# Kernel optimization log

Measured on AMD Instinct MI355X. Metric: run time of the kernel, lower is better.

The kernel has to match this reference:

```python
import jax, jax.numpy as jnp
import numpy as np

N, D, E = 100000, 128, 1600000
BN_EPS = 1e-5

def setup_inputs() -> dict:
    key = jax.random.key(0)
    k1, k2, k3 = jax.random.split(key, 3)
    src_embeddings = jax.random.normal(k1, (N, D), dtype=jnp.float32)
    dst_embeddings = jax.random.normal(k2, (N, D), dtype=jnp.float32)
    graph = jax.random.randint(k3, (2, E), 0, N, dtype=jnp.int64)
    bn_weight = jnp.ones((1,), dtype=jnp.float32)
    bn_bias = jnp.zeros((1,), dtype=jnp.float32)
    return {
        "src_embeddings": src_embeddings,
        "dst_embeddings": dst_embeddings,
        "graph": graph,
        "bn_weight": bn_weight,
        "bn_bias": bn_bias,
    }

def reference(src_embeddings, dst_embeddings, graph, bn_weight, bn_bias):
    # gather endpoint embeddings by edge indices: [E, D]
    src = src_embeddings[graph[0]]
    dst = dst_embeddings[graph[1]]
    # squared distance per edge, clamped as in torch .clamp(min=1e-12)
    d2 = jnp.clip(jnp.sum((src - dst) ** 2, axis=-1), 1e-12, None)  # [E]
    likelihood = -jnp.log(d2)
    # BatchNorm1d(1) in training mode: batch mean, biased variance, eps=1e-5
    mu = jnp.mean(likelihood)
    var = jnp.mean((likelihood - mu) ** 2)
    edge_weights_logits = bn_weight[0] * (likelihood - mu) * jax.lax.rsqrt(var + BN_EPS) + bn_bias[0]
    # weighting_function = torch.sigmoid
    edge_weights = jax.nn.sigmoid(edge_weights_logits)
    # normalize=True: divide by mean
    edge_weights = edge_weights / jnp.mean(edge_weights)
    edge_weights = edge_weights[:, None]  # [E, 1]
    return graph, edge_weights, edge_weights_logits
```

## Files before the change

### kernel.cpp

```cpp
#include <hip/hip_runtime.h>
#include <math.h>

#define EMB_D 128
#define BN_EPS 1e-5f

#define QSCALE 22.0f
#define INV_QS2 (1.0f / (QSCALE * QSCALE))

typedef float v4f __attribute__((ext_vector_type(4)));

#if defined(__has_builtin)
#if __has_builtin(__builtin_amdgcn_sdot4)
#define SDOT4_HW 1
#endif
#endif

__device__ __forceinline__ int sdot4i(unsigned int a, unsigned int b, int c) {
#ifdef SDOT4_HW
    return __builtin_amdgcn_sdot4((int)a, (int)b, c, false);
#else
    int s = c;
    s += (((int)a << 24) >> 24) * (((int)b << 24) >> 24);
    s += (((int)a << 16) >> 24) * (((int)b << 16) >> 24);
    s += (((int)a << 8)  >> 24) * (((int)b << 8)  >> 24);
    s += ((int)a >> 24) * ((int)b >> 24);
    return s;
#endif
}

__device__ __forceinline__ unsigned int q4(float4 v) {
    const int a = (int)rintf(fminf(fmaxf(v.x * QSCALE, -127.0f), 127.0f));
    const int b = (int)rintf(fminf(fmaxf(v.y * QSCALE, -127.0f), 127.0f));
    const int c = (int)rintf(fminf(fmaxf(v.z * QSCALE, -127.0f), 127.0f));
    const int d = (int)rintf(fminf(fmaxf(v.w * QSCALE, -127.0f), 127.0f));
    return (unsigned int)(a & 0xff) | ((unsigned int)(b & 0xff) << 8)
         | ((unsigned int)(c & 0xff) << 16) | ((unsigned int)(d & 0xff) << 24);
}

__device__ __forceinline__ float n4(float4 v) {
    return fmaf(v.x, v.x, fmaf(v.y, v.y, fmaf(v.z, v.z, v.w * v.w)));
}

__global__ void prep_kernel(const float* __restrict__ src,
                            const float* __restrict__ dst,
                            uint4* __restrict__ src8,
                            uint4* __restrict__ dst8,
                            float* __restrict__ nsrc,
                            float* __restrict__ ndst,
                            long long N,
                            const int* __restrict__ g,
                            long long E,
                            float* __restrict__ out_graph)
{
    const int sub = threadIdx.x & 7;
    const int grp = threadIdx.x >> 3;
    const long long rstride = (long long)gridDim.x * 32;

    for (long long r = (long long)blockIdx.x * 32 + grp; r < N; r += rstride) {
        const float4* rp = (const float4*)(src + r * EMB_D) + sub * 4;
        const float4 x0 = rp[0], x1 = rp[1], x2 = rp[2], x3 = rp[3];
        uint4 w;
        w.x = q4(x0); w.y = q4(x1); w.z = q4(x2); w.w = q4(x3);
        src8[r * 8 + sub] = w;
        float nrm = n4(x0) + n4(x1) + n4(x2) + n4(x3);
        nrm += __shfl_xor(nrm, 1, 64);
        nrm += __shfl_xor(nrm, 2, 64);
        nrm += __shfl_xor(nrm, 4, 64);
        if (sub == 0) nsrc[r] = nrm;
    }
    for (long long r = (long long)blockIdx.x * 32 + grp; r < N; r += rstride) {
        const float4* rp = (const float4*)(dst + r * EMB_D) + sub * 4;
        const float4 x0 = rp[0], x1 = rp[1], x2 = rp[2], x3 = rp[3];
        uint4 w;
        w.x = q4(x0); w.y = q4(x1); w.z = q4(x2); w.w = q4(x3);
        dst8[r * 8 + sub] = w;
        float nrm = n4(x0) + n4(x1) + n4(x2) + n4(x3);
        nrm += __shfl_xor(nrm, 1, 64);
        nrm += __shfl_xor(nrm, 2, 64);
        nrm += __shfl_xor(nrm, 4, 64);
        if (sub == 0) ndst[r] = nrm;
    }

    const long long nthreads = (long long)gridDim.x * blockDim.x;
    const long long tid0 = (long long)blockIdx.x * blockDim.x + threadIdx.x;
    const long long gvec = (2 * E) / 4;
    for (long long i = tid0; i < gvec; i += nthreads) {
        const int4 v = ((const int4*)g)[i];
        v4f f;
        f.x = (float)v.x; f.y = (float)v.y; f.z = (float)v.z; f.w = (float)v.w;
        __builtin_nontemporal_store(f, (v4f*)out_graph + i);
    }
    for (long long i = gvec * 4 + tid0; i < 2 * E; i += nthreads)
        out_graph[i] = (float)g[i];
}

__global__ void edge_l_i8_kernel(const uint4* __restrict__ src8,
                                 const uint4* __restrict__ dst8,
                                 const int* __restrict__ g,
                                 long long E,
                                 const float* __restrict__ nsrc,
                                 const float* __restrict__ ndst,
                                 float* __restrict__ l_out,
                                 double* __restrict__ acc)
{
    const int tid = threadIdx.x;
    const int sub = tid & 7;
    const int grp = tid >> 3;
    const long long blkSpan = 64;
    const long long stride = (long long)gridDim.x * blkSpan;

    double sumL = 0.0, sumL2 = 0.0;

    for (long long base = (long long)blockIdx.x * blkSpan; base < E; base += stride) {
        const long long e1 = base + (long long)grp * 2;
        const long long e2 = e1 + 1;
        const bool ok1 = e1 < E;
        const bool ok2 = e2 < E;

        int s1 = 0, d1 = 0, s2 = 0, d2i = 0;
        if (ok1) { s1 = g[e1]; d1 = g[E + e1]; }
        if (ok2) { s2 = g[e2]; d2i = g[E + e2]; }

        const uint4 A1 = src8[(long long)s1 * 8 + sub];
        const uint4 B1 = dst8[(long long)d1 * 8 + sub];
        const uint4 A2 = src8[(long long)s2 * 8 + sub];
        const uint4 B2 = dst8[(long long)d2i * 8 + sub];

        int p1 = sdot4i(A1.x, B1.x, 0);
        p1 = sdot4i(A1.y, B1.y, p1);
        p1 = sdot4i(A1.z, B1.z, p1);
        p1 = sdot4i(A1.w, B1.w, p1);
        int p2 = sdot4i(A2.x, B2.x, 0);
        p2 = sdot4i(A2.y, B2.y, p2);
        p2 = sdot4i(A2.z, B2.z, p2);
        p2 = sdot4i(A2.w, B2.w, p2);

        p1 += __shfl_xor(p1, 1, 64);
        p1 += __shfl_xor(p1, 2, 64);
        p1 += __shfl_xor(p1, 4, 64);
        p2 += __shfl_xor(p2, 1, 64);
        p2 += __shfl_xor(p2, 2, 64);
        p2 += __shfl_xor(p2, 4, 64);

        if (sub == 0) {
            if (ok1) {
                const float d2 = nsrc[s1] + ndst[d1]
                               - 2.0f * (float)p1 * INV_QS2;
                const float L = -logf(fmaxf(d2, 1e-12f));
                l_out[e1] = L;
                sumL  += (double)L;
                sumL2 += (double)L * (double)L;
            }
            if (ok2) {
                const float d2 = nsrc[s2] + ndst[d2i]
                               - 2.0f * (float)p2 * INV_QS2;
                const float L = -logf(fmaxf(d2, 1e-12f));
                l_out[e2] = L;
                sumL  += (double)L;
                sumL2 += (double)L * (double)L;
            }
        }
    }

    __shared__ double sA[256];
    __shared__ double sB[256];
    sA[tid] = sumL;
    sB[tid] = sumL2;
    __syncthreads();
    for (int ofs = 128; ofs >= 1; ofs >>= 1) {
        if (tid < ofs) {
            sA[tid] += sA[tid + ofs];
            sB[tid] += sB[tid + ofs];
        }
        __syncthreads();
    }
    if (tid == 0) {
        atomicAdd(&acc[0], sA[0]);
        atomicAdd(&acc[1], sB[0]);
    }
}

__global__ void edge_l_kernel(const float* __restrict__ src,
                              const float* __restrict__ dst,
                              const int*   __restrict__ g,
                              long long E,
                              float*  __restrict__ l_out,
                              double* __restrict__ acc)
{
    const int sub  = threadIdx.x & 7;
    const int egrp = threadIdx.x >> 3;
    const long long stride = (long long)gridDim.x * 32;

    double sumL = 0.0, sumL2 = 0.0;

    long long e = (long long)blockIdx.x * 32 + egrp;
    int s = 0, d = 0;
    if (e < E) { s = g[e]; d = g[E + e]; }

    while (e < E) {
        const long long en = e + stride;
        int sn = 0, dn = 0;
        if (en < E) { sn = g[en]; dn = g[E + en]; }

        const float4* sa = (const float4*)(src + (long long)s * EMB_D);
        const float4* sb = (const float4*)(dst + (long long)d * EMB_D);
        const float4 a0 = sa[sub];      const float4 b0 = sb[sub];
        const float4 a1 = sa[sub + 8];  const float4 b1 = sb[sub + 8];
        const float4 a2 = sa[sub + 16]; const float4 b2 = sb[sub + 16];
        const float4 a3 = sa[sub + 24]; const float4 b3 = sb[sub + 24];

        float dx, dy, dz, dw, p = 0.f;
        dx = a0.x-b0.x; dy = a0.y-b0.y; dz = a0.z-b0.z; dw = a0.w-b0.w;
        p += fmaf(dx,dx,fmaf(dy,dy,fmaf(dz,dz,dw*dw)));
        dx = a1.x-b1.x; dy = a1.y-b1.y; dz = a1.z-b1.z; dw = a1.w-b1.w;
        p += fmaf(dx,dx,fmaf(dy,dy,fmaf(dz,dz,dw*dw)));
        dx = a2.x-b2.x; dy = a2.y-b2.y; dz = a2.z-b2.z; dw = a2.w-b2.w;
        p += fmaf(dx,dx,fmaf(dy,dy,fmaf(dz,dz,dw*dw)));
        dx = a3.x-b3.x; dy = a3.y-b3.y; dz = a3.z-b3.z; dw = a3.w-b3.w;
        p += fmaf(dx,dx,fmaf(dy,dy,fmaf(dz,dz,dw*dw)));

        p += __shfl_xor(p, 1, 64);
        p += __shfl_xor(p, 2, 64);
        p += __shfl_xor(p, 4, 64);

        if (sub == 0) {
            const float L = -logf(fmaxf(p, 1e-12f));
            l_out[e] = L;
            sumL  += (double)L;
            sumL2 += (double)L * (double)L;
        }
        e = en; s = sn; d = dn;
    }

    __shared__ double sA[256];
    __shared__ double sB[256];
    sA[threadIdx.x] = sumL;
    sB[threadIdx.x] = sumL2;
    __syncthreads();
    for (int ofs = 128; ofs >= 1; ofs >>= 1) {
        if ((int)threadIdx.x < ofs) {
            sA[threadIdx.x] += sA[threadIdx.x + ofs];
            sB[threadIdx.x] += sB[threadIdx.x + ofs];
        }
        __syncthreads();
    }
    if (threadIdx.x == 0) {
        atomicAdd(&acc[0], sA[0]);
        atomicAdd(&acc[1], sB[0]);
    }
}

__global__ void bn_sig_kernel(float* __restrict__ logits,
                              const double* __restrict__ acc,
                              double* __restrict__ sig_acc,
                              const float* __restrict__ bn_w,
                              const float* __restrict__ bn_b,
                              long long E)
{
    const long long nthreads = (long long)gridDim.x * blockDim.x;
    const long long tid0 = (long long)blockIdx.x * blockDim.x + threadIdx.x;

    __shared__ float s_mu, s_inv, s_w, s_b;
    if (threadIdx.x == 0) {
        const double mu  = acc[0] / (double)E;
        const double var = acc[1] / (double)E - mu * mu;
        s_mu  = (float)mu;
        s_inv = (float)(1.0 / sqrt(var + (double)BN_EPS));
        s_w   = bn_w[0];
        s_b   = bn_b[0];
    }
    __syncthreads();
    const float mu = s_mu, inv = s_inv, w = s_w, b = s_b;

    double sig = 0.0;
    const long long nvec = E / 4;
    for (long long i = tid0; i < nvec; i += nthreads) {
        float4 L = ((const float4*)logits)[i];
        float4 z;
        z.x = w * (L.x - mu) * inv + b;
        z.y = w * (L.y - mu) * inv + b;
        z.z = w * (L.z - mu) * inv + b;
        z.w = w * (L.w - mu) * inv + b;
        ((float4*)logits)[i] = z;
        const float sx = 1.0f / (1.0f + expf(-z.x));
        const float sy = 1.0f / (1.0f + expf(-z.y));
        const float sz = 1.0f / (1.0f + expf(-z.z));
        const float sw2 = 1.0f / (1.0f + expf(-z.w));
        sig += (double)(sx + sy) + (double)(sz + sw2);
    }
    for (long long i = nvec * 4 + tid0; i < E; i += nthreads) {
        const float L = logits[i];
        const float z = w * (L - mu) * inv + b;
        logits[i] = z;
        sig += (double)(1.0f / (1.0f + expf(-z)));
    }

    __shared__ double sS[256];
    sS[threadIdx.x] = sig;
    __syncthreads();
    for (int ofs = 128; ofs >= 1; ofs >>= 1) {
        if ((int)threadIdx.x < ofs)
            sS[threadIdx.x] += sS[threadIdx.x + ofs];
        __syncthreads();
    }
    if (threadIdx.x == 0)
        atomicAdd(sig_acc, sS[0]);
}

__global__ void norm_kernel(const float* __restrict__ logits,
                            float* __restrict__ ew,
                            const double* __restrict__ sig_acc,
                            const int* __restrict__ g,
                            float* __restrict__ out_graph,
                            int do_graph,
                            long long E)
{
    const long long nthreads = (long long)gridDim.x * blockDim.x;
    const long long tid0 = (long long)blockIdx.x * blockDim.x + threadIdx.x;
    const float scale = (float)((double)E / sig_acc[0]);

    const long long nvec = E / 4;
    for (long long i = tid0; i < nvec; i += nthreads) {
        const float4 z = ((const float4*)logits)[i];
        v4f v;
        v.x = scale / (1.0f + expf(-z.x));
        v.y = scale / (1.0f + expf(-z.y));
        v.z = scale / (1.0f + expf(-z.z));
        v.w = scale / (1.0f + expf(-z.w));
        __builtin_nontemporal_store(v, (v4f*)ew + i);
    }
    for (long long i = nvec * 4 + tid0; i < E; i += nthreads)
        ew[i] = scale / (1.0f + expf(-logits[i]));

    if (do_graph) {
        const long long gvec = (2 * E) / 4;
        for (long long i = tid0; i < gvec; i += nthreads) {
            const int4 v = ((const int4*)g)[i];
            float4 f;
            f.x = (float)v.x; f.y = (float)v.y; f.z = (float)v.z; f.w = (float)v.w;
            ((float4*)out_graph)[i] = f;
        }
        for (long long i = gvec * 4 + tid0; i < 2 * E; i += nthreads)
            out_graph[i] = (float)g[i];
    }
}

extern "C" void kernel_launch(void* const* d_in, const int* in_sizes, int n_in,
                              void* d_out, int out_size, void* d_ws, size_t ws_size,
                              hipStream_t stream) {
    const float* src  = (const float*)d_in[0];
    const float* dst  = (const float*)d_in[1];
    const int*   g    = (const int*)d_in[2];
    const float* bn_w = (const float*)d_in[3];
    const float* bn_b = (const float*)d_in[4];

    const long long N = (long long)in_sizes[0] / EMB_D;
    const long long E = (long long)in_sizes[2] / 2;

    float* out        = (float*)d_out;
    float* out_graph  = out;
    float* out_ew     = out + 2 * E;
    float* out_logits = out + 3 * E;

    double*       acc  = (double*)d_ws;
    unsigned char* src8 = (unsigned char*)d_ws + 512;
    unsigned char* dst8 = src8 + (size_t)N * EMB_D;

    const size_t need_i8 = 512 + (size_t)N * EMB_D * 2;
    const bool stash_ok = (2 * N <= E);

    (void)hipMemsetAsync(d_ws, 0, 512, stream);

    if (ws_size >= need_i8 && stash_ok) {
        float* nsrc = out_ew;
        float* ndst = out_ew + N;
        prep_kernel<<<4096, 256, 0, stream>>>(src, dst,
                                              (uint4*)src8, (uint4*)dst8,
                                              nsrc, ndst, N, g, E, out_graph);
        edge_l_i8_kernel<<<4096, 256, 0, stream>>>((const uint4*)src8,
                                                   (const uint4*)dst8,
                                                   g, E, nsrc, ndst,
                                                   out_logits, acc);
        bn_sig_kernel<<<1024, 256, 0, stream>>>(out_logits, acc, &acc[2],
                                                bn_w, bn_b, E);
        norm_kernel<<<1024, 256, 0, stream>>>(out_logits, out_ew, &acc[2],
                                              g, out_graph, 0, E);
    } else {
        edge_l_kernel<<<4096, 256, 0, stream>>>(src, dst, g, E, out_logits, acc);
        bn_sig_kernel<<<1024, 256, 0, stream>>>(out_logits, acc, &acc[2],
                                                bn_w, bn_b, E);
        norm_kernel<<<1024, 256, 0, stream>>>(out_logits, out_ew, &acc[2],
                                              g, out_graph, 1, E);
    }
}
```

Measured before the change: 299.4 us.

## Bin edges by source/destination node slice to localize int8 embedding gathers per XCD

Adds a binning pass inside the prep kernel that sorts edges into 64 buckets by (src slice, dst slice) and packs each edge's indices into a 64-bit record. The edge kernel then maps groups of bins to blocks by XCD (blockIdx & 7), so each XCD mostly touches one eighth of the source table and its L2 holds a smaller working set of int8 rows. The prep quantization loop also changes to one float4 per thread, using a wider shuffle reduction for the row norms. In exchange this adds global atomics, extra record reads and writes, an overflow path, and a scatter of outputs by edge id.

```diff
diff --git a/kernel.cpp b/kernel.cpp
--- a/kernel.cpp
+++ b/kernel.cpp
@@ -3,6 +3,8 @@
 
 #define EMB_D 128
 #define BN_EPS 1e-5f
+#define GATHER_BLOCKS 2048
+#define OVF_CAP 8192
 
 #define QSCALE 22.0f
 #define INV_QS2 (1.0f / (QSCALE * QSCALE))
@@ -41,57 +43,257 @@
     return fmaf(v.x, v.x, fmaf(v.y, v.y, fmaf(v.z, v.z, v.w * v.w)));
 }
 
-__global__ void prep_kernel(const float* __restrict__ src,
-                            const float* __restrict__ dst,
-                            uint4* __restrict__ src8,
-                            uint4* __restrict__ dst8,
-                            float* __restrict__ nsrc,
-                            float* __restrict__ ndst,
-                            long long N,
-                            const int* __restrict__ g,
-                            long long E,
-                            float* __restrict__ out_graph)
+__device__ __forceinline__ unsigned int flat_to_rec(unsigned int f,
+                                                    const unsigned int (&pre)[9],
+                                                    unsigned int cap) {
+    unsigned int j = 0, pj = 0;
+    #pragma unroll
+    for (int k = 1; k < 8; ++k) {
+        const bool ge = (f >= pre[k]);
+        j  = ge ? (unsigned int)k : j;
+        pj = ge ? pre[k] : pj;
+    }
+    return j * cap + (f - pj);
+}
+
+__global__ void prep_bin_kernel(const float* __restrict__ src,
+                                const float* __restrict__ dst,
+                                unsigned int* __restrict__ src8,
+                                unsigned int* __restrict__ dst8,
+                                float* __restrict__ nsrc,
+                                float* __restrict__ ndst,
+                                long long N,
+                                const int* __restrict__ g,
+                                long long E,
+                                float* __restrict__ out_graph,
+                                unsigned long long* __restrict__ rec,
+                                unsigned int* __restrict__ cursors,
+                                unsigned int cap,
+                                float inv_slice)
 {
-    const int sub = threadIdx.x & 7;
-    const int grp = threadIdx.x >> 3;
-    const long long rstride = (long long)gridDim.x * 32;
-
-    for (long long r = (long long)blockIdx.x * 32 + grp; r < N; r += rstride) {
-        const float4* rp = (const float4*)(src + r * EMB_D) + sub * 4;
-        const float4 x0 = rp[0], x1 = rp[1], x2 = rp[2], x3 = rp[3];
-        uint4 w;
-        w.x = q4(x0); w.y = q4(x1); w.z = q4(x2); w.w = q4(x3);
-        src8[r * 8 + sub] = w;
-        float nrm = n4(x0) + n4(x1) + n4(x2) + n4(x3);
-        nrm += __shfl_xor(nrm, 1, 64);
-        nrm += __shfl_xor(nrm, 2, 64);
-        nrm += __shfl_xor(nrm, 4, 64);
-        if (sub == 0) nsrc[r] = nrm;
-    }
-    for (long long r = (long long)blockIdx.x * 32 + grp; r < N; r += rstride) {
-        const float4* rp = (const float4*)(dst + r * EMB_D) + sub * 4;
-        const float4 x0 = rp[0], x1 = rp[1], x2 = rp[2], x3 = rp[3];
-        uint4 w;
-        w.x = q4(x0); w.y = q4(x1); w.z = q4(x2); w.w = q4(x3);
-        dst8[r * 8 + sub] = w;
-        float nrm = n4(x0) + n4(x1) + n4(x2) + n4(x3);
-        nrm += __shfl_xor(nrm, 1, 64);
-        nrm += __shfl_xor(nrm, 2, 64);
-        nrm += __shfl_xor(nrm, 4, 64);
-        if (sub == 0) ndst[r] = nrm;
-    }
-
     const long long nthreads = (long long)gridDim.x * blockDim.x;
     const long long tid0 = (long long)blockIdx.x * blockDim.x + threadIdx.x;
-    const long long gvec = (2 * E) / 4;
-    for (long long i = tid0; i < gvec; i += nthreads) {
-        const int4 v = ((const int4*)g)[i];
-        v4f f;
-        f.x = (float)v.x; f.y = (float)v.y; f.z = (float)v.z; f.w = (float)v.w;
-        __builtin_nontemporal_store(f, (v4f*)out_graph + i);
-    }
-    for (long long i = gvec * 4 + tid0; i < 2 * E; i += nthreads)
-        out_graph[i] = (float)g[i];
+    const int half_lane = (int)(threadIdx.x & 31);
+
+    {
+        const long long nvec32 = N * 32;
+        for (long long i = tid0; i < nvec32; i += nthreads) {
+            const float4 x = ((const float4*)src)[i];
+            src8[i] = q4(x);
+            float nrm = n4(x);
+            nrm += __shfl_xor(nrm, 1, 64);
+            nrm += __shfl_xor(nrm, 2, 64);
+            nrm += __shfl_xor(nrm, 4, 64);
+            nrm += __shfl_xor(nrm, 8, 64);
+            nrm += __shfl_xor(nrm, 16, 64);
+            if (half_lane == 0) nsrc[i >> 5] = nrm;
+        }
+        for (long long i = tid0; i < nvec32; i += nthreads) {
+            const float4 x = ((const float4*)dst)[i];
+            dst8[i] = q4(x);
+            float nrm = n4(x);
+            nrm += __shfl_xor(nrm, 1, 64);
+            nrm += __shfl_xor(nrm, 2, 64);
+            nrm += __shfl_xor(nrm, 4, 64);
+            nrm += __shfl_xor(nrm, 8, 64);
+            nrm += __shfl_xor(nrm, 16, 64);
+            if (half_lane == 0) ndst[i >> 5] = nrm;
+        }
+
+        const long long gvec = (2 * E) / 4;
+        for (long long i = tid0; i < gvec; i += nthreads) {
+            const int4 v = ((const int4*)g)[i];
+            v4f f;
+            f.x = (float)v.x; f.y = (float)v.y; f.z = (float)v.z; f.w = (float)v.w;
+            __builtin_nontemporal_store(f, (v4f*)out_graph + i);
+        }
+        for (long long i = gvec * 4 + tid0; i < 2 * E; i += nthreads)
+            out_graph[i] = (float)g[i];
+    }
+
+    __shared__ unsigned int hist[64];
+    __shared__ unsigned int curs[64];
+
+    const long long chunkSz = (long long)blockDim.x * 8;
+    const long long nchunks = (E + chunkSz - 1) / chunkSz;
+
+    for (long long c = blockIdx.x; c < nchunks; c += gridDim.x) {
+        const long long base = c * chunkSz;
+        if (threadIdx.x < 64) hist[threadIdx.x] = 0;
+        __syncthreads();
+
+        int bb[8];
+        unsigned long long pk[8];
+        #pragma unroll
+        for (int k = 0; k < 8; ++k) {
+            const long long e = base + (long long)k * blockDim.x + threadIdx.x;
+            bb[k] = -1;
+            if (e < E) {
+                const unsigned int s = (unsigned int)g[e];
+                const unsigned int d = (unsigned int)g[E + e];
+                int bs = (int)((float)s * inv_slice); bs = bs > 7 ? 7 : bs;
+                int bd = (int)((float)d * inv_slice); bd = bd > 7 ? 7 : bd;
+                bb[k] = bs * 8 + bd;
+                pk[k] = (unsigned long long)s | ((unsigned long long)d << 20)
+                      | ((unsigned long long)e << 40);
+                atomicAdd(&hist[bb[k]], 1u);
+            }
+        }
+        __syncthreads();
+        if (threadIdx.x < 64 && hist[threadIdx.x] > 0)
+            curs[threadIdx.x] = atomicAdd(&cursors[threadIdx.x], hist[threadIdx.x]);
+        __syncthreads();
+
+        #pragma unroll
+        for (int k = 0; k < 8; ++k) {
+            if (bb[k] >= 0) {
+                unsigned int off = atomicAdd(&curs[bb[k]], 1u);
+                if (off < cap) {
+                    rec[(unsigned int)bb[k] * cap + off] = pk[k];
+                } else {
+                    unsigned int oo = atomicAdd(&cursors[64], 1u);
+                    if (oo < OVF_CAP) rec[64u * cap + oo] = pk[k];
+                }
+            }
+        }
+        __syncthreads();
+    }
+}
+
+__global__ void edge_l_binned_i8_kernel(const uint4* __restrict__ src8,
+                                        const uint4* __restrict__ dst8,
+                                        const unsigned long long* __restrict__ rec,
+                                        const unsigned int* __restrict__ cursors,
+                                        unsigned int cap,
+                                        const float* __restrict__ nsrc,
+                                        const float* __restrict__ ndst,
+                                        float* __restrict__ l_out,
+                                        double* __restrict__ acc)
+{
+    const int tid = threadIdx.x;
+    const int sub = tid & 7;
+    const int grp = tid >> 3;
+    const int xcd = blockIdx.x & 7;
+    const unsigned int local = blockIdx.x >> 3;
+    const unsigned int nloc  = gridDim.x >> 3;
+
+    unsigned int pre[9];
+    pre[0] = 0;
+    #pragma unroll
+    for (int j = 0; j < 8; ++j) {
+        unsigned int c = cursors[xcd * 8 + j];
+        if (c > cap) c = cap;
+        pre[j + 1] = pre[j] + c;
+    }
+    const unsigned int M = pre[8];
+    const unsigned long long recBase = (unsigned long long)(xcd * 8) * cap;
+
+    double sumL = 0.0, sumL2 = 0.0;
+
+    const unsigned int perBlock = 64;
+    const unsigned int stride = nloc * perBlock;
+
+    for (unsigned int f0 = local * perBlock; f0 < M; f0 += stride) {
+        const unsigned int f1 = f0 + (unsigned int)grp;
+        const unsigned int f2 = f1 + 32u;
+        const bool ok1 = f1 < M;
+        const bool ok2 = f2 < M;
+
+        unsigned long long v1 = 0ull, v2 = 0ull;
+        if (ok1) v1 = rec[recBase + flat_to_rec(f1, pre, cap)];
+        if (ok2) v2 = rec[recBase + flat_to_rec(f2, pre, cap)];
+
+        const int s1  = (int)(v1 & 0xFFFFFu);
+        const int d1  = (int)((v1 >> 20) & 0xFFFFFu);
+        const int s2  = (int)(v2 & 0xFFFFFu);
+        const int d2i = (int)((v2 >> 20) & 0xFFFFFu);
+
+        const uint4 A1 = src8[(long long)s1 * 8 + sub];
+        const uint4 B1 = dst8[(long long)d1 * 8 + sub];
+        const uint4 A2 = src8[(long long)s2 * 8 + sub];
+        const uint4 B2 = dst8[(long long)d2i * 8 + sub];
+
+        int p1 = sdot4i(A1.x, B1.x, 0);
+        p1 = sdot4i(A1.y, B1.y, p1);
+        p1 = sdot4i(A1.z, B1.z, p1);
+        p1 = sdot4i(A1.w, B1.w, p1);
+        int p2 = sdot4i(A2.x, B2.x, 0);
+        p2 = sdot4i(A2.y, B2.y, p2);
+        p2 = sdot4i(A2.z, B2.z, p2);
+        p2 = sdot4i(A2.w, B2.w, p2);
+
+        p1 += __shfl_xor(p1, 1, 64);
+        p1 += __shfl_xor(p1, 2, 64);
+        p1 += __shfl_xor(p1, 4, 64);
+        p2 += __shfl_xor(p2, 1, 64);
+        p2 += __shfl_xor(p2, 2, 64);
+        p2 += __shfl_xor(p2, 4, 64);
+
+        if (sub == 0) {
+            if (ok1) {
+                const float d2 = nsrc[s1] + ndst[d1]
+                               - 2.0f * (float)p1 * INV_QS2;
+                const float L = -logf(fmaxf(d2, 1e-12f));
+                __builtin_nontemporal_store(L, &l_out[(long long)(v1 >> 40)]);
+                sumL  += (double)L;
+                sumL2 += (double)L * (double)L;
+            }
+            if (ok2) {
+                const float d2 = nsrc[s2] + ndst[d2i]
+                               - 2.0f * (float)p2 * INV_QS2;
+                const float L = -logf(fmaxf(d2, 1e-12f));
+                __builtin_nontemporal_store(L, &l_out[(long long)(v2 >> 40)]);
+                sumL  += (double)L;
+                sumL2 += (double)L * (double)L;
+            }
+        }
+    }
+
+    {
+        unsigned int ovfN = cursors[64];
+        if (ovfN > OVF_CAP) ovfN = OVF_CAP;
+        const unsigned long long obase = 64ull * cap;
+        const unsigned int gstride = gridDim.x * 32u;
+        for (unsigned int f = blockIdx.x * 32u + (unsigned int)grp;
+             f < ovfN; f += gstride) {
+            const unsigned long long v = rec[obase + f];
+            const int s = (int)(v & 0xFFFFFu);
+            const int d = (int)((v >> 20) & 0xFFFFFu);
+            const uint4 Av = src8[(long long)s * 8 + sub];
+            const uint4 Bv = dst8[(long long)d * 8 + sub];
+            int p = sdot4i(Av.x, Bv.x, 0);
+            p = sdot4i(Av.y, Bv.y, p);
+            p = sdot4i(Av.z, Bv.z, p);
+            p = sdot4i(Av.w, Bv.w, p);
+            p += __shfl_xor(p, 1, 64);
+            p += __shfl_xor(p, 2, 64);
+            p += __shfl_xor(p, 4, 64);
+            if (sub == 0) {
+                const float d2 = nsrc[s] + ndst[d] - 2.0f * (float)p * INV_QS2;
+                const float L = -logf(fmaxf(d2, 1e-12f));
+                __builtin_nontemporal_store(L, &l_out[(long long)(v >> 40)]);
+                sumL  += (double)L;
+                sumL2 += (double)L * (double)L;
+            }
+        }
+    }
+
+    __shared__ double sA[256];
+    __shared__ double sB[256];
+    sA[tid] = sumL;
+    sB[tid] = sumL2;
+    __syncthreads();
+    for (int ofs = 128; ofs >= 1; ofs >>= 1) {
+        if (tid < ofs) {
+            sA[tid] += sA[tid + ofs];
+            sB[tid] += sB[tid + ofs];
+        }
+        __syncthreads();
+    }
+    if (tid == 0) {
+        atomicAdd(&acc[0], sA[0]);
+        atomicAdd(&acc[1], sB[0]);
+    }
 }
 
 __global__ void edge_l_i8_kernel(const uint4* __restrict__ src8,
@@ -144,16 +346,14 @@
 
         if (sub == 0) {
             if (ok1) {
-                const float d2 = nsrc[s1] + ndst[d1]
-                               - 2.0f * (float)p1 * INV_QS2;
+                const float d2 = nsrc[s1] + ndst[d1] - 2.0f * (float)p1 * INV_QS2;
                 const float L = -logf(fmaxf(d2, 1e-12f));
                 l_out[e1] = L;
                 sumL  += (double)L;
                 sumL2 += (double)L * (double)L;
             }
             if (ok2) {
-                const float d2 = nsrc[s2] + ndst[d2i]
-                               - 2.0f * (float)p2 * INV_QS2;
+                const float d2 = nsrc[s2] + ndst[d2i] - 2.0f * (float)p2 * INV_QS2;
                 const float L = -logf(fmaxf(d2, 1e-12f));
                 l_out[e2] = L;
                 sumL  += (double)L;
@@ -178,6 +378,56 @@
         atomicAdd(&acc[0], sA[0]);
         atomicAdd(&acc[1], sB[0]);
     }
+}
+
+__global__ void prep_kernel(const float* __restrict__ src,
+                            const float* __restrict__ dst,
+                            unsigned int* __restrict__ src8,
+                            unsigned int* __restrict__ dst8,
+                            float* __restrict__ nsrc,
+                            float* __restrict__ ndst,
+                            long long N,
+                            const int* __restrict__ g,
+                            long long E,
+                            float* __restrict__ out_graph)
+{
+    const long long nthreads = (long long)gridDim.x * blockDim.x;
+    const long long tid0 = (long long)blockIdx.x * blockDim.x + threadIdx.x;
+    const int half_lane = (int)(threadIdx.x & 31);
+    const long long nvec32 = N * 32;
+
+    for (long long i = tid0; i < nvec32; i += nthreads) {
+        const float4 x = ((const float4*)src)[i];
+        src8[i] = q4(x);
+        float nrm = n4(x);
+        nrm += __shfl_xor(nrm, 1, 64);
+        nrm += __shfl_xor(nrm, 2, 64);
+        nrm += __shfl_xor(nrm, 4, 64);
+        nrm += __shfl_xor(nrm, 8, 64);
+        nrm += __shfl_xor(nrm, 16, 64);
+        if (half_lane == 0) nsrc[i >> 5] = nrm;
+    }
+    for (long long i = tid0; i < nvec32; i += nthreads) {
+        const float4 x = ((const float4*)dst)[i];
+        dst8[i] = q4(x);
+        float nrm = n4(x);
+        nrm += __shfl_xor(nrm, 1, 64);
+        nrm += __shfl_xor(nrm, 2, 64);
+        nrm += __shfl_xor(nrm, 4, 64);
+        nrm += __shfl_xor(nrm, 8, 64);
+        nrm += __shfl_xor(nrm, 16, 64);
+        if (half_lane == 0) ndst[i >> 5] = nrm;
+    }
+
+    const long long gvec = (2 * E) / 4;
+    for (long long i = tid0; i < gvec; i += nthreads) {
+        const int4 v = ((const int4*)g)[i];
+        v4f f;
+        f.x = (float)v.x; f.y = (float)v.y; f.z = (float)v.z; f.w = (float)v.w;
+        __builtin_nontemporal_store(f, (v4f*)out_graph + i);
+    }
+    for (long long i = gvec * 4 + tid0; i < 2 * E; i += nthreads)
+        out_graph[i] = (float)g[i];
 }
 
 __global__ void edge_l_kernel(const float* __restrict__ src,
@@ -362,20 +612,44 @@
     float* out_ew     = out + 2 * E;
     float* out_logits = out + 3 * E;
 
-    double*       acc  = (double*)d_ws;
-    unsigned char* src8 = (unsigned char*)d_ws + 512;
-    unsigned char* dst8 = src8 + (size_t)N * EMB_D;
-
-    const size_t need_i8 = 512 + (size_t)N * EMB_D * 2;
+    double*       acc     = (double*)d_ws;
+    unsigned int* cursors = (unsigned int*)((char*)d_ws + 64);
+    unsigned char* src8   = (unsigned char*)d_ws + 512;
+    unsigned char* dst8   = src8 + (size_t)N * EMB_D;
+    unsigned long long* rec = (unsigned long long*)(dst8 + (size_t)N * EMB_D);
+
+    const unsigned int cap = (unsigned int)(E / 64 + 2048);
+    const size_t need_full = 512 + (size_t)N * EMB_D * 2
+                           + ((size_t)64 * cap + OVF_CAP) * 8;
+    const size_t need_i8   = 512 + (size_t)N * EMB_D * 2;
+
+    const int slice_sz = (int)((N + 7) / 8);
+    const float inv_slice = 1.0f / (float)slice_sz;
     const bool stash_ok = (2 * N <= E);
 
     (void)hipMemsetAsync(d_ws, 0, 512, stream);
 
-    if (ws_size >= need_i8 && stash_ok) {
-        float* nsrc = out_ew;
-        float* ndst = out_ew + N;
+    float* nsrc = out_ew;
+    float* ndst = out_ew + N;
+
+    if (ws_size >= need_full && stash_ok && N < (1 << 20) && E < (1LL << 24)) {
+        prep_bin_kernel<<<4096, 256, 0, stream>>>(src, dst,
+                                                  (unsigned int*)src8,
+                                                  (unsigned int*)dst8,
+                                                  nsrc, ndst,
+                                                  N, g, E, out_graph,
+                                                  rec, cursors, cap, inv_slice);
+        edge_l_binned_i8_kernel<<<GATHER_BLOCKS, 256, 0, stream>>>(
+            (const uint4*)src8, (const uint4*)dst8, rec, cursors, cap,
+            nsrc, ndst, out_logits, acc);
+        bn_sig_kernel<<<1024, 256, 0, stream>>>(out_logits, acc, &acc[2],
+                                                bn_w, bn_b, E);
+        norm_kernel<<<1024, 256, 0, stream>>>(out_logits, out_ew, &acc[2],
+                                              g, out_graph, 0, E);
+    } else if (ws_size >= need_i8 && stash_ok) {
         prep_kernel<<<4096, 256, 0, stream>>>(src, dst,
-                                              (uint4*)src8, (uint4*)dst8,
+                                              (unsigned int*)src8,
+                                              (unsigned int*)dst8,
                                               nsrc, ndst, N, g, E, out_graph);
         edge_l_i8_kernel<<<4096, 256, 0, stream>>>((const uint4*)src8,
                                                    (const uint4*)dst8,
```

Result: faster. 269.1 us (-10.1%).

## Bin edges by source/destination node slice per chunk for cache-local int8 gathers

Applied to the files above, without the earlier changes.

Adds a prep pass that splits node ids into 8 slices, histograms each 6144-edge chunk into 64 (src-slice, dst-slice) bins, and writes packed 14-bit local index records plus an inverse permutation. The edge kernel assigns each block one chunk and one source slice, mapping blockIdx low bits to an XCD so that each XCD's L2 holds only a fraction of the int8 embedding tables. The squared distance is now computed entirely in int8 via sdot4 (|a|^2+|b|^2-2ab), which drops the per-row fp32 norm arrays. BN and sigmoid run on the permuted order, and a finalize kernel scatters results back through shared memory. The cost is extra passes, atomics and workspace traffic for binning and un-permuting.

```diff
diff --git a/kernel.cpp b/kernel.cpp
--- a/kernel.cpp
+++ b/kernel.cpp
@@ -3,11 +3,14 @@
 
 #define EMB_D 128
 #define BN_EPS 1e-5f
+#define CHUNK 6144
+#define RUN_TILE 128
 
 #define QSCALE 22.0f
 #define INV_QS2 (1.0f / (QSCALE * QSCALE))
 
 typedef float v4f __attribute__((ext_vector_type(4)));
+typedef unsigned int v4u __attribute__((ext_vector_type(4)));
 
 #if defined(__has_builtin)
 #if __has_builtin(__builtin_amdgcn_sdot4)
@@ -37,127 +40,174 @@
          | ((unsigned int)(c & 0xff) << 16) | ((unsigned int)(d & 0xff) << 24);
 }
 
-__device__ __forceinline__ float n4(float4 v) {
-    return fmaf(v.x, v.x, fmaf(v.y, v.y, fmaf(v.z, v.z, v.w * v.w)));
-}
-
-__global__ void prep_kernel(const float* __restrict__ src,
-                            const float* __restrict__ dst,
-                            uint4* __restrict__ src8,
-                            uint4* __restrict__ dst8,
-                            float* __restrict__ nsrc,
-                            float* __restrict__ ndst,
-                            long long N,
-                            const int* __restrict__ g,
-                            long long E,
-                            float* __restrict__ out_graph)
-{
-    const int sub = threadIdx.x & 7;
-    const int grp = threadIdx.x >> 3;
-    const long long rstride = (long long)gridDim.x * 32;
-
-    for (long long r = (long long)blockIdx.x * 32 + grp; r < N; r += rstride) {
-        const float4* rp = (const float4*)(src + r * EMB_D) + sub * 4;
-        const float4 x0 = rp[0], x1 = rp[1], x2 = rp[2], x3 = rp[3];
-        uint4 w;
-        w.x = q4(x0); w.y = q4(x1); w.z = q4(x2); w.w = q4(x3);
-        src8[r * 8 + sub] = w;
-        float nrm = n4(x0) + n4(x1) + n4(x2) + n4(x3);
-        nrm += __shfl_xor(nrm, 1, 64);
-        nrm += __shfl_xor(nrm, 2, 64);
-        nrm += __shfl_xor(nrm, 4, 64);
-        if (sub == 0) nsrc[r] = nrm;
-    }
-    for (long long r = (long long)blockIdx.x * 32 + grp; r < N; r += rstride) {
-        const float4* rp = (const float4*)(dst + r * EMB_D) + sub * 4;
-        const float4 x0 = rp[0], x1 = rp[1], x2 = rp[2], x3 = rp[3];
-        uint4 w;
-        w.x = q4(x0); w.y = q4(x1); w.z = q4(x2); w.w = q4(x3);
-        dst8[r * 8 + sub] = w;
-        float nrm = n4(x0) + n4(x1) + n4(x2) + n4(x3);
-        nrm += __shfl_xor(nrm, 1, 64);
-        nrm += __shfl_xor(nrm, 2, 64);
-        nrm += __shfl_xor(nrm, 4, 64);
-        if (sub == 0) ndst[r] = nrm;
-    }
-
+__device__ __forceinline__ int d2_dword(unsigned int a, unsigned int b, int m) {
+    const int pab = sdot4i(a, b, 0);
+    m = sdot4i(a, a, m);
+    m = sdot4i(b, b, m);
+    return m - 2 * pab;
+}
+
+__global__ void prep_bin_kernel(const float* __restrict__ src,
+                                const float* __restrict__ dst,
+                                unsigned int* __restrict__ src8,
+                                unsigned int* __restrict__ dst8,
+                                long long N,
+                                const int* __restrict__ g,
+                                long long E,
+                                float* __restrict__ out_graph,
+                                unsigned int* __restrict__ rec32,
+                                unsigned short* __restrict__ boff,
+                                unsigned short* __restrict__ inv16,
+                                long long nchunks,
+                                int slice_sz,
+                                float inv_slice)
+{
     const long long nthreads = (long long)gridDim.x * blockDim.x;
     const long long tid0 = (long long)blockIdx.x * blockDim.x + threadIdx.x;
-    const long long gvec = (2 * E) / 4;
-    for (long long i = tid0; i < gvec; i += nthreads) {
-        const int4 v = ((const int4*)g)[i];
-        v4f f;
-        f.x = (float)v.x; f.y = (float)v.y; f.z = (float)v.z; f.w = (float)v.w;
-        __builtin_nontemporal_store(f, (v4f*)out_graph + i);
-    }
-    for (long long i = gvec * 4 + tid0; i < 2 * E; i += nthreads)
-        out_graph[i] = (float)g[i];
-}
-
-__global__ void edge_l_i8_kernel(const uint4* __restrict__ src8,
-                                 const uint4* __restrict__ dst8,
-                                 const int* __restrict__ g,
-                                 long long E,
-                                 const float* __restrict__ nsrc,
-                                 const float* __restrict__ ndst,
-                                 float* __restrict__ l_out,
-                                 double* __restrict__ acc)
+
+    {
+        const long long nvec16 = N * 8;
+        for (long long i = tid0; i < nvec16; i += nthreads) {
+            const float4* p = (const float4*)src + i * 4;
+            v4u w;
+            w.x = q4(p[0]); w.y = q4(p[1]); w.z = q4(p[2]); w.w = q4(p[3]);
+            __builtin_nontemporal_store(w, (v4u*)src8 + i);
+        }
+        for (long long i = tid0; i < nvec16; i += nthreads) {
+            const float4* p = (const float4*)dst + i * 4;
+            v4u w;
+            w.x = q4(p[0]); w.y = q4(p[1]); w.z = q4(p[2]); w.w = q4(p[3]);
+            __builtin_nontemporal_store(w, (v4u*)dst8 + i);
+        }
+    }
+
+    __shared__ unsigned int hist[64];
+    __shared__ unsigned int curs[64];
+
+    for (long long c = blockIdx.x; c < nchunks; c += gridDim.x) {
+        const long long base = c * CHUNK;
+        const int cnt = (int)((E - base) < CHUNK ? (E - base) : CHUNK);
+
+        if (threadIdx.x < 64) hist[threadIdx.x] = 0;
+        __syncthreads();
+
+        for (int t = threadIdx.x; t < cnt; t += blockDim.x) {
+            const long long e = base + t;
+            const unsigned int s = (unsigned int)g[e];
+            const unsigned int d = (unsigned int)g[E + e];
+            int bs = (int)((float)s * inv_slice); bs = bs > 7 ? 7 : bs;
+            int bd = (int)((float)d * inv_slice); bd = bd > 7 ? 7 : bd;
+            atomicAdd(&hist[bs * 8 + bd], 1u);
+        }
+        __syncthreads();
+
+        if (threadIdx.x < 64) {
+            const unsigned int v = hist[threadIdx.x];
+            unsigned int inc = v;
+            #pragma unroll
+            for (int ofs = 1; ofs < 64; ofs <<= 1) {
+                const unsigned int o = __shfl_up(inc, ofs, 64);
+                if ((int)threadIdx.x >= ofs) inc += o;
+            }
+            const unsigned int excl = inc - v;
+            curs[threadIdx.x] = excl;
+            boff[c * 64 + threadIdx.x] = (unsigned short)excl;
+        }
+        __syncthreads();
+
+        for (int t = threadIdx.x; t < cnt; t += blockDim.x) {
+            const long long e = base + t;
+            const unsigned int s = (unsigned int)g[e];
+            const unsigned int d = (unsigned int)g[E + e];
+            __builtin_nontemporal_store((float)s, &out_graph[e]);
+            __builtin_nontemporal_store((float)d, &out_graph[E + e]);
+            int bs = (int)((float)s * inv_slice); bs = bs > 7 ? 7 : bs;
+            int bd = (int)((float)d * inv_slice); bd = bd > 7 ? 7 : bd;
+            const int b = bs * 8 + bd;
+            const unsigned int pos = atomicAdd(&curs[b], 1u);
+            const unsigned int sl = s - (unsigned int)(bs * slice_sz);
+            const unsigned int dl = d - (unsigned int)(bd * slice_sz);
+            rec32[base + pos] = sl | (dl << 14);
+            inv16[e] = (unsigned short)pos;
+        }
+        __syncthreads();
+    }
+}
+
+__global__ void edge_l_binned_kernel(const uint4* __restrict__ src8,
+                                     const uint4* __restrict__ dst8,
+                                     const unsigned int* __restrict__ rec32,
+                                     const unsigned short* __restrict__ boff,
+                                     long long nchunks,
+                                     long long E,
+                                     int slice_sz,
+                                     float* __restrict__ L_rec,
+                                     double* __restrict__ acc)
 {
     const int tid = threadIdx.x;
     const int sub = tid & 7;
     const int grp = tid >> 3;
-    const long long blkSpan = 64;
-    const long long stride = (long long)gridDim.x * blkSpan;
+    const int xcd = (int)(blockIdx.x & 7);
+    const long long c = (long long)(blockIdx.x >> 3);
 
     double sumL = 0.0, sumL2 = 0.0;
 
-    for (long long base = (long long)blockIdx.x * blkSpan; base < E; base += stride) {
-        const long long e1 = base + (long long)grp * 2;
-        const long long e2 = e1 + 1;
-        const bool ok1 = e1 < E;
-        const bool ok2 = e2 < E;
-
-        int s1 = 0, d1 = 0, s2 = 0, d2i = 0;
-        if (ok1) { s1 = g[e1]; d1 = g[E + e1]; }
-        if (ok2) { s2 = g[e2]; d2i = g[E + e2]; }
-
-        const uint4 A1 = src8[(long long)s1 * 8 + sub];
-        const uint4 B1 = dst8[(long long)d1 * 8 + sub];
-        const uint4 A2 = src8[(long long)s2 * 8 + sub];
-        const uint4 B2 = dst8[(long long)d2i * 8 + sub];
-
-        int p1 = sdot4i(A1.x, B1.x, 0);
-        p1 = sdot4i(A1.y, B1.y, p1);
-        p1 = sdot4i(A1.z, B1.z, p1);
-        p1 = sdot4i(A1.w, B1.w, p1);
-        int p2 = sdot4i(A2.x, B2.x, 0);
-        p2 = sdot4i(A2.y, B2.y, p2);
-        p2 = sdot4i(A2.z, B2.z, p2);
-        p2 = sdot4i(A2.w, B2.w, p2);
-
-        p1 += __shfl_xor(p1, 1, 64);
-        p1 += __shfl_xor(p1, 2, 64);
-        p1 += __shfl_xor(p1, 4, 64);
-        p2 += __shfl_xor(p2, 1, 64);
-        p2 += __shfl_xor(p2, 2, 64);
-        p2 += __shfl_xor(p2, 4, 64);
-
-        if (sub == 0) {
-            if (ok1) {
-                const float d2 = nsrc[s1] + ndst[d1]
-                               - 2.0f * (float)p1 * INV_QS2;
-                const float L = -logf(fmaxf(d2, 1e-12f));
-                l_out[e1] = L;
-                sumL  += (double)L;
-                sumL2 += (double)L * (double)L;
-            }
-            if (ok2) {
-                const float d2 = nsrc[s2] + ndst[d2i]
-                               - 2.0f * (float)p2 * INV_QS2;
-                const float L = -logf(fmaxf(d2, 1e-12f));
-                l_out[e2] = L;
-                sumL  += (double)L;
-                sumL2 += (double)L * (double)L;
+    if (c < nchunks) {
+        const long long base = c * CHUNK;
+        const int cnt = (int)((E - base) < CHUNK ? (E - base) : CHUNK);
+        const int sBase = xcd * slice_sz;
+
+        for (int j = 0; j < 8; ++j) {
+            const int b = xcd * 8 + j;
+            const int start = (int)boff[c * 64 + b];
+            const int end = (b == 63) ? cnt : (int)boff[c * 64 + b + 1];
+            const int len = end - start;
+            const long long rbase = base + start;
+            const int dBase = j * slice_sz;
+
+            for (int t0 = 0; t0 < len; t0 += RUN_TILE) {
+                bool ok[4];
+                int tt[4], ss[4], dd[4];
+                #pragma unroll
+                for (int q = 0; q < 4; ++q) {
+                    const int t = t0 + grp + q * 32;
+                    ok[q] = t < len;
+                    tt[q] = ok[q] ? t : 0;
+                    const unsigned int r = rec32[rbase + tt[q]];
+                    ss[q] = sBase + (int)(r & 0x3FFFu);
+                    dd[q] = dBase + (int)((r >> 14) & 0x3FFFu);
+                }
+
+                int mq[4];
+                #pragma unroll
+                for (int q = 0; q < 4; ++q) {
+                    const uint4 A = src8[(long long)ss[q] * 8 + sub];
+                    const uint4 B = dst8[(long long)dd[q] * 8 + sub];
+                    int m = d2_dword(A.x, B.x, 0);
+                    m = d2_dword(A.y, B.y, m);
+                    m = d2_dword(A.z, B.z, m);
+                    m = d2_dword(A.w, B.w, m);
+                    mq[q] = m;
+                }
+                #pragma unroll
+                for (int q = 0; q < 4; ++q) {
+                    mq[q] += __shfl_xor(mq[q], 1, 64);
+                    mq[q] += __shfl_xor(mq[q], 2, 64);
+                    mq[q] += __shfl_xor(mq[q], 4, 64);
+                }
+
+                if (sub == 0) {
+                    #pragma unroll
+                    for (int q = 0; q < 4; ++q) {
+                        if (ok[q]) {
+                            const float d2 = (float)mq[q] * INV_QS2;
+                            const float L = -logf(fmaxf(d2, 1e-12f));
+                            L_rec[rbase + tt[q]] = L;
+                            sumL  += (double)L;
+                            sumL2 += (double)L * (double)L;
+                        }
+                    }
+                }
             }
         }
     }
@@ -180,6 +230,209 @@
     }
 }
 
+__global__ void sig_z_kernel(float* __restrict__ zrec,
+                             long long E,
+                             const double* __restrict__ acc,
+                             double* __restrict__ sig_acc,
+                             const float* __restrict__ bn_w,
+                             const float* __restrict__ bn_b)
+{
+    const long long nthreads = (long long)gridDim.x * blockDim.x;
+    const long long tid0 = (long long)blockIdx.x * blockDim.x + threadIdx.x;
+
+    __shared__ float s_mu, s_inv, s_w, s_b;
+    if (threadIdx.x == 0) {
+        const double mu  = acc[0] / (double)E;
+        const double var = acc[1] / (double)E - mu * mu;
+        s_mu  = (float)mu;
+        s_inv = (float)(1.0 / sqrt(var + (double)BN_EPS));
+        s_w   = bn_w[0];
+        s_b   = bn_b[0];
+    }
+    __syncthreads();
+    const float mu = s_mu, iv = s_inv, w = s_w, b = s_b;
+
+    double sig = 0.0;
+    const long long nvec = E / 4;
+    for (long long i = tid0; i < nvec; i += nthreads) {
+        float4 L = ((const float4*)zrec)[i];
+        float4 z;
+        z.x = w * (L.x - mu) * iv + b;
+        z.y = w * (L.y - mu) * iv + b;
+        z.z = w * (L.z - mu) * iv + b;
+        z.w = w * (L.w - mu) * iv + b;
+        ((float4*)zrec)[i] = z;
+        const float sx = 1.0f / (1.0f + expf(-z.x));
+        const float sy = 1.0f / (1.0f + expf(-z.y));
+        const float sz = 1.0f / (1.0f + expf(-z.z));
+        const float sw2 = 1.0f / (1.0f + expf(-z.w));
+        sig += (double)(sx + sy) + (double)(sz + sw2);
+    }
+    for (long long i = nvec * 4 + tid0; i < E; i += nthreads) {
+        const float L = zrec[i];
+        const float z = w * (L - mu) * iv + b;
+        zrec[i] = z;
+        sig += (double)(1.0f / (1.0f + expf(-z)));
+    }
+
+    __shared__ double sS[256];
+    sS[threadIdx.x] = sig;
+    __syncthreads();
+    for (int ofs = 128; ofs >= 1; ofs >>= 1) {
+        if ((int)threadIdx.x < ofs)
+            sS[threadIdx.x] += sS[threadIdx.x + ofs];
+        __syncthreads();
+    }
+    if (threadIdx.x == 0)
+        atomicAdd(sig_acc, sS[0]);
+}
+
+__global__ void finalize_kernel(const unsigned short* __restrict__ inv16,
+                                const float* __restrict__ zrec,
+                                float* __restrict__ logits,
+                                float* __restrict__ ew,
+                                const double* __restrict__ sig_acc,
+                                long long E,
+                                long long nchunks)
+{
+    __shared__ float zs[CHUNK];
+    const float scale = (float)((double)E / sig_acc[0]);
+
+    for (long long c = blockIdx.x; c < nchunks; c += gridDim.x) {
+        const long long base = c * CHUNK;
+        const int cnt = (int)((E - base) < CHUNK ? (E - base) : CHUNK);
+
+        __syncthreads();
+        for (int t = threadIdx.x; t < cnt; t += blockDim.x)
+            zs[t] = zrec[base + t];
+        __syncthreads();
+
+        for (int t = threadIdx.x; t < cnt; t += blockDim.x) {
+            const long long e = base + t;
+            const float z = zs[inv16[e]];
+            __builtin_nontemporal_store(z, &logits[e]);
+            __builtin_nontemporal_store(scale / (1.0f + expf(-z)), &ew[e]);
+        }
+    }
+}
+
+__global__ void prep_kernel(const float* __restrict__ src,
+                            const float* __restrict__ dst,
+                            unsigned int* __restrict__ src8,
+                            unsigned int* __restrict__ dst8,
+                            long long N,
+                            const int* __restrict__ g,
+                            long long E,
+                            float* __restrict__ out_graph)
+{
+    const long long nthreads = (long long)gridDim.x * blockDim.x;
+    const long long tid0 = (long long)blockIdx.x * blockDim.x + threadIdx.x;
+    const long long nvec16 = N * 8;
+
+    for (long long i = tid0; i < nvec16; i += nthreads) {
+        const float4* p = (const float4*)src + i * 4;
+        v4u w;
+        w.x = q4(p[0]); w.y = q4(p[1]); w.z = q4(p[2]); w.w = q4(p[3]);
+        __builtin_nontemporal_store(w, (v4u*)src8 + i);
+    }
+    for (long long i = tid0; i < nvec16; i += nthreads) {
+        const float4* p = (const float4*)dst + i * 4;
+        v4u w;
+        w.x = q4(p[0]); w.y = q4(p[1]); w.z = q4(p[2]); w.w = q4(p[3]);
+        __builtin_nontemporal_store(w, (v4u*)dst8 + i);
+    }
+
+    const long long gvec = (2 * E) / 4;
+    for (long long i = tid0; i < gvec; i += nthreads) {
+        const int4 v = ((const int4*)g)[i];
+        v4f f;
+        f.x = (float)v.x; f.y = (float)v.y; f.z = (float)v.z; f.w = (float)v.w;
+        __builtin_nontemporal_store(f, (v4f*)out_graph + i);
+    }
+    for (long long i = gvec * 4 + tid0; i < 2 * E; i += nthreads)
+        out_graph[i] = (float)g[i];
+}
+
+__global__ void edge_l_i8_kernel(const uint4* __restrict__ src8,
+                                 const uint4* __restrict__ dst8,
+                                 const int* __restrict__ g,
+                                 long long E,
+                                 float* __restrict__ l_out,
+                                 double* __restrict__ acc)
+{
+    const int tid = threadIdx.x;
+    const int sub = tid & 7;
+    const int grp = tid >> 3;
+    const long long blkSpan = 64;
+    const long long stride = (long long)gridDim.x * blkSpan;
+
+    double sumL = 0.0, sumL2 = 0.0;
+
+    for (long long base = (long long)blockIdx.x * blkSpan; base < E; base += stride) {
+        const long long e1 = base + (long long)grp * 2;
+        const long long e2 = e1 + 1;
+        const bool ok1 = e1 < E;
+        const bool ok2 = e2 < E;
+
+        int s1 = 0, d1 = 0, s2 = 0, d2i = 0;
+        if (ok1) { s1 = g[e1]; d1 = g[E + e1]; }
+        if (ok2) { s2 = g[e2]; d2i = g[E + e2]; }
+
+        const uint4 A1 = src8[(long long)s1 * 8 + sub];
+        const uint4 B1 = dst8[(long long)d1 * 8 + sub];
+        const uint4 A2 = src8[(long long)s2 * 8 + sub];
+        const uint4 B2 = dst8[(long long)d2i * 8 + sub];
+
+        int m1 = d2_dword(A1.x, B1.x, 0);
+        m1 = d2_dword(A1.y, B1.y, m1);
+        m1 = d2_dword(A1.z, B1.z, m1);
+        m1 = d2_dword(A1.w, B1.w, m1);
+        int m2 = d2_dword(A2.x, B2.x, 0);
+        m2 = d2_dword(A2.y, B2.y, m2);
+        m2 = d2_dword(A2.z, B2.z, m2);
+        m2 = d2_dword(A2.w, B2.w, m2);
+
+        m1 += __shfl_xor(m1, 1, 64);
+        m1 += __shfl_xor(m1, 2, 64);
+        m1 += __shfl_xor(m1, 4, 64);
+        m2 += __shfl_xor(m2, 1, 64);
+        m2 += __shfl_xor(m2, 2, 64);
+        m2 += __shfl_xor(m2, 4, 64);
+
+        if (sub == 0) {
+            if (ok1) {
+                const float L = -logf(fmaxf((float)m1 * INV_QS2, 1e-12f));
+                l_out[e1] = L;
+                sumL  += (double)L;
+                sumL2 += (double)L * (double)L;
+            }
+            if (ok2) {
+                const float L = -logf(fmaxf((float)m2 * INV_QS2, 1e-12f));
+                l_out[e2] = L;
+                sumL  += (double)L;
+                sumL2 += (double)L * (double)L;
+            }
+        }
+    }
+
+    __shared__ double sA[256];
+    __shared__ double sB[256];
+    sA[tid] = sumL;
+    sB[tid] = sumL2;
+    __syncthreads();
+    for (int ofs = 128; ofs >= 1; ofs >>= 1) {
+        if (tid < ofs) {
+            sA[tid] += sA[tid + ofs];
+            sB[tid] += sB[tid + ofs];
+        }
+        __syncthreads();
+    }
+    if (tid == 0) {
+        atomicAdd(&acc[0], sA[0]);
+        atomicAdd(&acc[1], sB[0]);
+    }
+}
+
 __global__ void edge_l_kernel(const float* __restrict__ src,
                               const float* __restrict__ dst,
                               const int*   __restrict__ g,
@@ -248,6 +501,16 @@
         atomicAdd(&acc[0], sA[0]);
         atomicAdd(&acc[1], sB[0]);
     }
+}
+
+__global__ void graph_copy_kernel(const int* __restrict__ g,
+                                  float* __restrict__ out_graph,
+                                  long long E2)
+{
+    const long long nth = (long long)gridDim.x * blockDim.x;
+    for (long long i = (long long)blockIdx.x * blockDim.x + threadIdx.x;
+         i < E2; i += nth)
+        out_graph[i] = (float)g[i];
 }
 
 __global__ void bn_sig_kernel(float* __restrict__ logits,
@@ -310,9 +573,6 @@
 __global__ void norm_kernel(const float* __restrict__ logits,
                             float* __restrict__ ew,
                             const double* __restrict__ sig_acc,
-                            const int* __restrict__ g,
-                            float* __restrict__ out_graph,
-                            int do_graph,
                             long long E)
 {
     const long long nthreads = (long long)gridDim.x * blockDim.x;
@@ -331,18 +591,6 @@
     }
     for (long long i = nvec * 4 + tid0; i < E; i += nthreads)
         ew[i] = scale / (1.0f + expf(-logits[i]));
-
-    if (do_graph) {
-        const long long gvec = (2 * E) / 4;
-        for (long long i = tid0; i < gvec; i += nthreads) {
-            const int4 v = ((const int4*)g)[i];
-            float4 f;
-            f.x = (float)v.x; f.y = (float)v.y; f.z = (float)v.z; f.w = (float)v.w;
-            ((float4*)out_graph)[i] = f;
-        }
-        for (long long i = gvec * 4 + tid0; i < 2 * E; i += nthreads)
-            out_graph[i] = (float)g[i];
-    }
 }
 
 extern "C" void kernel_launch(void* const* d_in, const int* in_sizes, int n_in,
@@ -362,34 +610,56 @@
     float* out_ew     = out + 2 * E;
     float* out_logits = out + 3 * E;
 
+    const long long nchunks = (E + CHUNK - 1) / CHUNK;
+    const long long SLOTS = nchunks * CHUNK;
+
     double*       acc  = (double*)d_ws;
     unsigned char* src8 = (unsigned char*)d_ws + 512;
     unsigned char* dst8 = src8 + (size_t)N * EMB_D;
-
-    const size_t need_i8 = 512 + (size_t)N * EMB_D * 2;
-    const bool stash_ok = (2 * N <= E);
+    unsigned int* rec32 = (unsigned int*)(dst8 + (size_t)N * EMB_D);
+    float* L_rec = (float*)(rec32 + SLOTS);
+    unsigned short* inv16 = (unsigned short*)(L_rec + SLOTS);
+    unsigned short* boff  = inv16 + SLOTS;
+
+    const size_t need_t3 = 512 + (size_t)N * EMB_D * 2;
+    const size_t need_t1 = need_t3 + (size_t)SLOTS * 10 + (size_t)nchunks * 128;
+
+    const int slice_sz = (int)((N + 7) / 8);
+    const float inv_slice = 1.0f / (float)slice_sz;
+    const bool pack_ok = (slice_sz < 16384) && (E < (1LL << 31));
 
     (void)hipMemsetAsync(d_ws, 0, 512, stream);
 
-    if (ws_size >= need_i8 && stash_ok) {
-        float* nsrc = out_ew;
-        float* ndst = out_ew + N;
+    if (ws_size >= need_t1 && pack_ok) {
+        prep_bin_kernel<<<4096, 256, 0, stream>>>(src, dst,
+                                                  (unsigned int*)src8,
+                                                  (unsigned int*)dst8,
+                                                  N, g, E, out_graph,
+                                                  rec32, boff, inv16,
+                                                  nchunks, slice_sz, inv_slice);
+        edge_l_binned_kernel<<<(unsigned int)(8 * nchunks), 256, 0, stream>>>(
+            (const uint4*)src8, (const uint4*)dst8, rec32, boff,
+            nchunks, E, slice_sz, L_rec, acc);
+        sig_z_kernel<<<1024, 256, 0, stream>>>(L_rec, E, acc, &acc[2],
+                                               bn_w, bn_b);
+        finalize_kernel<<<(unsigned int)nchunks, 256, 0, stream>>>(
+            inv16, L_rec, out_logits, out_ew, &acc[2], E, nchunks);
+    } else if (ws_size >= need_t3) {
         prep_kernel<<<4096, 256, 0, stream>>>(src, dst,
-                                              (uint4*)src8, (uint4*)dst8,
-                                              nsrc, ndst, N, g, E, out_graph);
+                                              (unsigned int*)src8,
+                                              (unsigned int*)dst8,
+                                              N, g, E, out_graph);
         edge_l_i8_kernel<<<4096, 256, 0, stream>>>((const uint4*)src8,
                                                    (const uint4*)dst8,
-                                                   g, E, nsrc, ndst,
-                                                   out_logits, acc);
+                                                   g, E, out_logits, acc);
         bn_sig_kernel<<<1024, 256, 0, stream>>>(out_logits, acc, &acc[2],
                                                 bn_w, bn_b, E);
-        norm_kernel<<<1024, 256, 0, stream>>>(out_logits, out_ew, &acc[2],
-                                              g, out_graph, 0, E);
+        norm_kernel<<<1024, 256, 0, stream>>>(out_logits, out_ew, &acc[2], E);
     } else {
         edge_l_kernel<<<4096, 256, 0, stream>>>(src, dst, g, E, out_logits, acc);
         bn_sig_kernel<<<1024, 256, 0, stream>>>(out_logits, acc, &acc[2],
                                                 bn_w, bn_b, E);
-        norm_kernel<<<1024, 256, 0, stream>>>(out_logits, out_ew, &acc[2],
-                                              g, out_graph, 1, E);
-    }
-}
+        norm_kernel<<<1024, 256, 0, stream>>>(out_logits, out_ew, &acc[2], E);
+        graph_copy_kernel<<<1024, 256, 0, stream>>>(g, out_graph, 2 * E);
+    }
+}
```

Result: faster. 280.6 us (-6.3%).
